# Kernel tuning notes

Hardware: AMD Instinct MI355X
Metric: run time of the kernel (lower is better)

## Reference

```python
import jax, jax.numpy as jnp
import numpy as np

DIM = 256
D_STATE = 16
D_CONV = 4
EXPAND = 2
D_INNER = DIM * EXPAND          # 512
DT_RANK = DIM // 16             # 16


def _dwconv(x_bcl, w, b, pad):
    # depthwise 1d conv; x_bcl: (B, C, L), w: (C, 1, K)
    out = jax.lax.conv_general_dilated(
        x_bcl, w, window_strides=(1,), padding=[pad],
        feature_group_count=x_bcl.shape[1],
        dimension_numbers=('NCH', 'OIH', 'NCH'))
    return out + b[None, :, None]


def _forward(x, ln_w, ln_b, W_in, conv_w, conv_b, W_xproj, W_dt, b_dt,
             A_log, D_ssm, W_outp, c1_w, c1_b, c2_w, c2_b, c3_w, c3_b,
             W_out, b_out, W_skip, b_skip):
    Bsz, C = x.shape[:2]
    img_dims = x.shape[2:]
    L = int(np.prod(img_dims))
    xf = x.reshape(Bsz, C, L).transpose(0, 2, 1)          # (B, L, C)
    # LayerNorm over channel dim
    mu = jnp.mean(xf, axis=-1, keepdims=True)
    var = jnp.var(xf, axis=-1, keepdims=True)
    xn = (xf - mu) / jnp.sqrt(var + 1e-5) * ln_w + ln_b   # (B, L, C)

    # ---------------- Mamba block ----------------
    xz = xn @ W_in.T                                      # (B, L, 2*Di)
    xi, z = jnp.split(xz, 2, axis=-1)
    k = conv_w.shape[-1]
    # causal depthwise conv (pad left d_conv-1, truncate to L), then silu
    xc = _dwconv(xi.transpose(0, 2, 1), conv_w, conv_b, (k - 1, 0))
    xc = jax.nn.silu(xc).transpose(0, 2, 1)               # (B, L, Di)
    x_dbl = xc @ W_xproj.T                                # (B, L, dt_rank + 2*N)
    dt = x_dbl[..., :DT_RANK]
    B_s = x_dbl[..., DT_RANK:DT_RANK + D_STATE]           # (B, L, N)
    C_s = x_dbl[..., DT_RANK + D_STATE:]                  # (B, L, N)
    delta = jax.nn.softplus(dt @ W_dt.T + b_dt)           # (B, L, Di)
    A = -jnp.exp(A_log)                                   # (Di, N)
    dA = jnp.exp(delta[..., None] * A)                    # (B, L, Di, N)
    dBu = (delta * xc)[..., None] * B_s[:, :, None, :]    # (B, L, Di, N)

    def step(h, inp):
        dA_t, dBu_t, c_t = inp
        h = dA_t * h + dBu_t                              # (B, Di, N)
        y = jnp.einsum('bdn,bn->bd', h, c_t)
        return h, y

    h0 = jnp.zeros((Bsz, D_INNER, D_STATE), dtype=x.dtype)
    _, ys = jax.lax.scan(
        step, h0,
        (dA.transpose(1, 0, 2, 3), dBu.transpose(1, 0, 2, 3), C_s.transpose(1, 0, 2)))
    y = ys.transpose(1, 0, 2) + D_ssm * xc                # (B, L, Di)
    y = y * jax.nn.silu(z)
    x_ssm = y @ W_outp.T                                  # (B, L, C)

    # ---------------- multi-scale depthwise convs ----------------
    xnT = xn.transpose(0, 2, 1)                           # (B, C, L)

    def msconv(w, b):
        kk = w.shape[-1]
        return jax.nn.silu(_dwconv(xnT, w, b, (kk // 2, kk // 2))).transpose(0, 2, 1)

    combined = x_ssm + msconv(c1_w, c1_b) + msconv(c2_w, c2_b) + msconv(c3_w, c3_b)
    out = combined @ W_out.T + b_out + xn @ W_skip.T + b_skip
    out = out.transpose(0, 2, 1).reshape(x.shape)
    return out + x


def setup_inputs() -> dict:
    key = jax.random.key(0)
    ks = jax.random.split(key, 12)

    def rn(k, shape, s=0.02):
        return jax.random.normal(k, shape, dtype=jnp.float32) * s

    return {
        'x': jax.random.normal(ks[0], (2, DIM, 64, 64), dtype=jnp.float32),
        'ln_w': jnp.ones((DIM,), jnp.float32),
        'ln_b': jnp.zeros((DIM,), jnp.float32),
        'W_in': rn(ks[1], (2 * D_INNER, DIM)),
        'conv_w': rn(ks[2], (D_INNER, 1, D_CONV), 0.1),
        'conv_b': jnp.zeros((D_INNER,), jnp.float32),
        'W_xproj': rn(ks[3], (DT_RANK + 2 * D_STATE, D_INNER)),
        'W_dt': rn(ks[4], (D_INNER, DT_RANK), 0.1),
        'b_dt': jnp.full((D_INNER,), -4.0, jnp.float32),  # softplus(-4) ~ 0.018, stable dt
        'A_log': jnp.log(jnp.broadcast_to(
            jnp.arange(1, D_STATE + 1, dtype=jnp.float32), (D_INNER, D_STATE))),
        'D_ssm': jnp.ones((D_INNER,), jnp.float32),
        'W_outp': rn(ks[5], (DIM, D_INNER)),
        'c1_w': rn(ks[6], (DIM, 1, 3), 0.1),
        'c1_b': jnp.zeros((DIM,), jnp.float32),
        'c2_w': rn(ks[7], (DIM, 1, 5), 0.1),
        'c2_b': jnp.zeros((DIM,), jnp.float32),
        'c3_w': rn(ks[8], (DIM, 1, 7), 0.1),
        'c3_b': jnp.zeros((DIM,), jnp.float32),
        'W_out': rn(ks[9], (DIM, DIM)),
        'b_out': jnp.zeros((DIM,), jnp.float32),
        'W_skip': rn(ks[10], (DIM, DIM)),
        'b_skip': jnp.zeros((DIM,), jnp.float32),
    }


def reference(x, ln_w, ln_b, W_in, conv_w, conv_b, W_xproj, W_dt, b_dt,
              A_log, D_ssm, W_outp, c1_w, c1_b, c2_w, c2_b, c3_w, c3_b,
              W_out, b_out, W_skip, b_skip):
    return _forward(x, ln_w, ln_b, W_in, conv_w, conv_b, W_xproj, W_dt, b_dt,
                    A_log, D_ssm, W_outp, c1_w, c1_b, c2_w, c2_b, c3_w, c3_b,
                    W_out, b_out, W_skip, b_skip)
```

## Files before the change

### kernel.cpp

```cpp
#include <hip/hip_runtime.h>
#include <hip/hip_bf16.h>
#include <math.h>
#include <cstddef>

#define BSZ 2
#define DM 256
#define LSEQ 4096
#define DIN 512
#define DXZ 1024
#define DS 16
#define RANK 16
#define GXP 48
#define LC 32
#define NC 128

typedef __attribute__((ext_vector_type(8))) short short8;
typedef __attribute__((ext_vector_type(4))) float f32x4;
struct bf4 { __hip_bfloat16 v[4]; };

__device__ __forceinline__ float silu_f(float x){ return x / (1.f + __expf(-x)); }
__device__ __forceinline__ float softplus_f(float x){ return fmaxf(x, 0.f) + log1pf(__expf(-fabsf(x))); }
__device__ __forceinline__ float b2f(__hip_bfloat16 v){ return __bfloat162float(v); }
__device__ __forceinline__ __hip_bfloat16 f2b(float v){ return __float2bfloat16(v); }

__device__ __forceinline__ void gl_lds16(const void* g, void* s){
    __builtin_amdgcn_global_load_lds((const __attribute__((address_space(1))) void*)g,
                                     (__attribute__((address_space(3))) void*)s, 16, 0, 0);
}

__global__ __launch_bounds__(256) void k_ln(const float* __restrict__ x,
                                            const float* __restrict__ lnw,
                                            const float* __restrict__ lnb,
                                            __hip_bfloat16* __restrict__ xnb){
    __shared__ float tile[DM * 33];
    __shared__ float rsum[8][32], rsq[8][32];
    __shared__ float mu_s[32], rs_s[32];
    int b  = blockIdx.x >> 7;
    int l0 = (blockIdx.x & 127) << 5;
    int tid = threadIdx.x;
    const float* xb = x + (size_t)b * DM * LSEQ;
    int lls = tid & 31, chi = tid >> 5;
    for (int cc = 0; cc < 32; ++cc){
        int c = cc * 8 + chi;
        tile[c * 33 + lls] = xb[(size_t)c * LSEQ + l0 + lls];
    }
    __syncthreads();
    int part = tid >> 5, l = tid & 31;
    float s = 0.f, sq = 0.f;
    for (int i = 0; i < 32; ++i){
        float v = tile[(part * 32 + i) * 33 + l];
        s += v; sq += v * v;
    }
    rsum[part][l] = s; rsq[part][l] = sq;
    __syncthreads();
    if (tid < 32){
        float ts = 0.f, tq = 0.f;
        for (int p = 0; p < 8; ++p){ ts += rsum[p][tid]; tq += rsq[p][tid]; }
        float mu  = ts * (1.f / DM);
        float var = tq * (1.f / DM) - mu * mu;
        mu_s[tid] = mu;
        rs_s[tid] = rsqrtf(var + 1e-5f);
    }
    __syncthreads();
    int c0 = tid & 63, lh = tid >> 6;
    for (int i = 0; i < 8; ++i){
        int ll = lh + 4 * i;
        float mu = mu_s[ll], rs = rs_s[ll];
        __hip_bfloat16* orow = xnb + (size_t)(b * LSEQ + l0 + ll) * 512;
        for (int j = 0; j < 4; ++j){
            int c = c0 + 64 * j;
            orow[c] = f2b((tile[c * 33 + ll] - mu) * rs * lnw[c] + lnb[c]);
        }
    }
}

__global__ __launch_bounds__(256) void k_cvtw(const float* __restrict__ W_in, const float* __restrict__ W_xproj,
                                              const float* __restrict__ W_outp, const float* __restrict__ W_out,
                                              const float* __restrict__ W_skip, const float* __restrict__ b_out,
                                              const float* __restrict__ b_skip,
                                              __hip_bfloat16* __restrict__ Winb, __hip_bfloat16* __restrict__ Wxpb,
                                              __hip_bfloat16* __restrict__ Wopb, __hip_bfloat16* __restrict__ Wcb,
                                              float* __restrict__ bc){
    int i0 = blockIdx.x * 256 + threadIdx.x;
    const int T = 256 * 256;
    for (int j = i0; j < 1024 * 256; j += T) Winb[j] = f2b(W_in[j]);
    for (int j = i0; j < 64 * 512; j += T){
        int r = j >> 9;
        Wxpb[j] = f2b(r < GXP ? W_xproj[r * 512 + (j & 511)] : 0.f);
    }
    for (int j = i0; j < 256 * 512; j += T) Wopb[j] = f2b(W_outp[j]);
    for (int j = i0; j < 256 * 512; j += T){
        int n = j >> 9, k = j & 511;
        Wcb[j] = f2b(k < 256 ? W_out[n * 256 + k] : W_skip[n * 256 + (k - 256)]);
    }
    if (i0 < 256) bc[i0] = b_out[i0] + b_skip[i0];
}

template<int EPI>
__global__ __launch_bounds__(256) void k_mgemm(const __hip_bfloat16* __restrict__ A, int lda,
                                               const __hip_bfloat16* __restrict__ W,
                                               const float* __restrict__ bias,
                                               void* __restrict__ Cv, int ldc,
                                               int N, int K){
    __shared__ __align__(16) __hip_bfloat16 As[128 * 64];
    __shared__ __align__(16) __hip_bfloat16 Ws[64 * 64];
    const int tid = threadIdx.x;
    const int wave = tid >> 6, lane = tid & 63;
    const int brow = blockIdx.x * 128, bcol = blockIdx.y * 64;
    const int wm = wave >> 1, wn = wave & 1;

    const int a_row = lane >> 3;
    const int a_chk = lane & 7;
    const int a_scol = ((a_chk ^ a_row) * 8);

    const int lrow = lane & 15;
    const int kc = lane >> 4;
    const int r7 = lrow & 7;

    f32x4 acc[4][2] = {};

    for (int k0 = 0; k0 < K; k0 += 64){
#pragma unroll
        for (int j = 0; j < 4; ++j){
            int seg = wave * 4 + j;
            const __hip_bfloat16* src = A + (size_t)(brow + seg * 8 + a_row) * lda + k0 + a_scol;
            gl_lds16(src, &As[seg * 512]);
        }
#pragma unroll
        for (int j = 0; j < 2; ++j){
            int seg = wave * 2 + j;
            const __hip_bfloat16* src = W + (size_t)(bcol + seg * 8 + a_row) * K + k0 + a_scol;
            gl_lds16(src, &Ws[seg * 512]);
        }
        __syncthreads();
#pragma unroll
        for (int kk = 0; kk < 2; ++kk){
            int kchunk = kk * 4 + kc;
            short8 af[4], bfr[2];
#pragma unroll
            for (int mi = 0; mi < 4; ++mi){
                int row = wm * 64 + mi * 16 + lrow;
                af[mi] = *(const short8*)&As[row * 64 + ((kchunk ^ r7) * 8)];
            }
#pragma unroll
            for (int ni = 0; ni < 2; ++ni){
                int row = wn * 32 + ni * 16 + lrow;
                bfr[ni] = *(const short8*)&Ws[row * 64 + ((kchunk ^ r7) * 8)];
            }
#pragma unroll
            for (int mi = 0; mi < 4; ++mi)
#pragma unroll
                for (int ni = 0; ni < 2; ++ni)
                    acc[mi][ni] = __builtin_amdgcn_mfma_f32_16x16x32_bf16(af[mi], bfr[ni], acc[mi][ni], 0, 0, 0);
        }
        __syncthreads();
    }

#pragma unroll
    for (int ni = 0; ni < 2; ++ni){
        int n = bcol + wn * 32 + ni * 16 + lrow;
        if (n >= N) continue;
        float bv = (EPI & 1) ? bias[n] : 0.f;
#pragma unroll
        for (int mi = 0; mi < 4; ++mi){
            int m0 = brow + wm * 64 + mi * 16 + kc * 4;
#pragma unroll
            for (int r = 0; r < 4; ++r){
                float v = acc[mi][ni][r] + bv;
                if (EPI & 8) ((__hip_bfloat16*)Cv)[(size_t)(m0 + r) * ldc + n] = f2b(v);
                else         ((float*)Cv)[(size_t)(m0 + r) * ldc + n] = v;
            }
        }
    }
}

__global__ __launch_bounds__(256) void k_dtgemm(const float* __restrict__ A, int lda,
                                                const float* __restrict__ Wt,
                                                const float* __restrict__ bias,
                                                __hip_bfloat16* __restrict__ C, int ldc){
    __shared__ float As[16][68];
    __shared__ float Ws[16][68];
    int bm = blockIdx.x * 64, bn = blockIdx.y * 64;
    int tid = threadIdx.x;
    int a_m = tid >> 2, a_k = (tid & 3) * 4;
    int tx = tid & 15, ty = tid >> 4;
    float acc[4][4] = {};
    {
        float4 av = *(const float4*)(A + (size_t)(bm + a_m) * lda + a_k);
        As[a_k + 0][a_m] = av.x; As[a_k + 1][a_m] = av.y;
        As[a_k + 2][a_m] = av.z; As[a_k + 3][a_m] = av.w;
        float4 wv = *(const float4*)(Wt + (size_t)(bn + a_m) * 16 + a_k);
        Ws[a_k + 0][a_m] = wv.x; Ws[a_k + 1][a_m] = wv.y;
        Ws[a_k + 2][a_m] = wv.z; Ws[a_k + 3][a_m] = wv.w;
        __syncthreads();
#pragma unroll
        for (int k = 0; k < 16; ++k){
            float4 a4 = *(const float4*)&As[k][ty * 4];
            float4 b4 = *(const float4*)&Ws[k][tx * 4];
            acc[0][0] += a4.x * b4.x; acc[0][1] += a4.x * b4.y; acc[0][2] += a4.x * b4.z; acc[0][3] += a4.x * b4.w;
            acc[1][0] += a4.y * b4.x; acc[1][1] += a4.y * b4.y; acc[1][2] += a4.y * b4.z; acc[1][3] += a4.y * b4.w;
            acc[2][0] += a4.z * b4.x; acc[2][1] += a4.z * b4.y; acc[2][2] += a4.z * b4.z; acc[2][3] += a4.z * b4.w;
            acc[3][0] += a4.w * b4.x; acc[3][1] += a4.w * b4.y; acc[3][2] += a4.w * b4.z; acc[3][3] += a4.w * b4.w;
        }
    }
    int n = bn + tx * 4;
    float4 bb = *(const float4*)(bias + n);
#pragma unroll
    for (int i = 0; i < 4; ++i){
        int m = bm + ty * 4 + i;
        __hip_bfloat16* cp = C + (size_t)m * ldc + n;
        cp[0] = f2b(softplus_f(acc[i][0] + bb.x));
        cp[1] = f2b(softplus_f(acc[i][1] + bb.y));
        cp[2] = f2b(softplus_f(acc[i][2] + bb.z));
        cp[3] = f2b(softplus_f(acc[i][3] + bb.w));
    }
}

__global__ __launch_bounds__(256) void k_conv(const __hip_bfloat16* __restrict__ xz,
                                              const float* __restrict__ cw,
                                              const float* __restrict__ cb,
                                              __hip_bfloat16* __restrict__ xc){
    int idx = blockIdx.x * 256 + threadIdx.x;
    int d4 = (idx & 127) * 4;
    int bl = idx >> 7;
    int l  = bl & (LSEQ - 1);
    const __hip_bfloat16* base = xz + (size_t)bl * DXZ + d4;
    float4 bias = *(const float4*)(cb + d4);
    float acc[4] = {bias.x, bias.y, bias.z, bias.w};
    float4 w0 = *(const float4*)(cw + (d4 + 0) * 4);
    float4 w1 = *(const float4*)(cw + (d4 + 1) * 4);
    float4 w2 = *(const float4*)(cw + (d4 + 2) * 4);
    float4 w3 = *(const float4*)(cw + (d4 + 3) * 4);
    const float* wj[4] = {(const float*)&w0, (const float*)&w1, (const float*)&w2, (const float*)&w3};
#pragma unroll
    for (int t = 0; t < 4; ++t){
        int ls = l - (3 - t);
        if (ls >= 0){
            bf4 v = *(const bf4*)(base - (size_t)(3 - t) * DXZ);
#pragma unroll
            for (int j = 0; j < 4; ++j) acc[j] += wj[j][t] * b2f(v.v[j]);
        }
    }
    bf4 o;
#pragma unroll
    for (int j = 0; j < 4; ++j) o.v[j] = f2b(silu_f(acc[j]));
    *(bf4*)(xc + (size_t)bl * DIN + d4) = o;
}

__global__ __launch_bounds__(512) void k_scan1(const __hip_bfloat16* __restrict__ delta,
                                               const __hip_bfloat16* __restrict__ xc,
                                               const float* __restrict__ xdbl,
                                               const float* __restrict__ A_log,
                                               float* __restrict__ Acar,
                                               float* __restrict__ Bcar){
    int bx = blockIdx.x;
    int dh = bx & 1;
    int c  = (bx >> 1) & (NC - 1);
    int b  = bx >> 8;
    int tid = threadIdx.x;
    int dloc = tid >> 1, nh = tid & 1;
    int d = dh * 256 + dloc;
    int n0 = nh * 8;
    __shared__ float Bs[LC][DS];
    {
        int t = tid >> 4, n = tid & 15;
        Bs[t][n] = xdbl[(size_t)(b * LSEQ + c * LC + t) * GXP + RANK + n];
    }
    __syncthreads();
    float Av[8];
    float a1 = -__expf(A_log[d * 16]);
    bool fast = true;
#pragma unroll
    for (int j = 0; j < 8; ++j){
        Av[j] = -__expf(A_log[d * 16 + n0 + j]);
        fast = fast && (fabsf(Av[j] - (float)(n0 + j + 1) * a1) <= 1e-4f * fabsf(Av[j]) + 1e-7f);
    }
    float ap[8], ac[8];
#pragma unroll
    for (int j = 0; j < 8; ++j){ ap[j] = 1.f; ac[j] = 0.f; }
    const __hip_bfloat16* dp = delta + (size_t)(b * LSEQ + c * LC) * DIN + d;
    const __hip_bfloat16* xp = xc    + (size_t)(b * LSEQ + c * LC) * DIN + d;
    if (fast){
        for (int t = 0; t < LC; ++t){
            float de = b2f(dp[(size_t)t * DIN]);
            float u  = de * b2f(xp[(size_t)t * DIN]);
            float p  = __expf(de * a1);
            float p2 = p * p, p4 = p2 * p2, p8 = p4 * p4;
            float da = nh ? p8 * p : p;
#pragma unroll
            for (int j = 0; j < 8; ++j){
                ap[j] *= da;
                ac[j] = da * ac[j] + u * Bs[t][n0 + j];
                da *= p;
            }
        }
    } else {
        for (int t = 0; t < LC; ++t){
            float de = b2f(dp[(size_t)t * DIN]);
            float u  = de * b2f(xp[(size_t)t * DIN]);
#pragma unroll
            for (int j = 0; j < 8; ++j){
                float da = __expf(de * Av[j]);
                ap[j] *= da;
                ac[j] = da * ac[j] + u * Bs[t][n0 + j];
            }
        }
    }
    size_t o = (size_t)c * (BSZ * DIN * 16) + (size_t)(b * DIN + d) * 16 + n0;
    *(float4*)(Acar + o)     = make_float4(ap[0], ap[1], ap[2], ap[3]);
    *(float4*)(Acar + o + 4) = make_float4(ap[4], ap[5], ap[6], ap[7]);
    *(float4*)(Bcar + o)     = make_float4(ac[0], ac[1], ac[2], ac[3]);
    *(float4*)(Bcar + o + 4) = make_float4(ac[4], ac[5], ac[6], ac[7]);
}

__global__ __launch_bounds__(128) void k_scan2(const float* __restrict__ Acar,
                                               const float* __restrict__ Bcar,
                                               float* __restrict__ hinit){
    int idx = blockIdx.x * 128 + threadIdx.x;
    const int STRIDE = BSZ * DIN * 16;
    float h = 0.f;
    for (int c = 0; c < NC; c += 4){
        size_t o0 = (size_t)c * STRIDE + idx;
        float a0 = Acar[o0], b0 = Bcar[o0];
        float a1 = Acar[o0 + STRIDE], b1 = Bcar[o0 + STRIDE];
        float a2 = Acar[o0 + 2 * STRIDE], b2 = Bcar[o0 + 2 * STRIDE];
        float a3 = Acar[o0 + 3 * STRIDE], b3 = Bcar[o0 + 3 * STRIDE];
        hinit[o0] = h;               h = a0 * h + b0;
        hinit[o0 + STRIDE] = h;      h = a1 * h + b1;
        hinit[o0 + 2 * STRIDE] = h;  h = a2 * h + b2;
        hinit[o0 + 3 * STRIDE] = h;  h = a3 * h + b3;
    }
}

__global__ __launch_bounds__(512) void k_scan3(const __hip_bfloat16* __restrict__ delta,
                                               const __hip_bfloat16* __restrict__ xc,
                                               const __hip_bfloat16* __restrict__ xz,
                                               const float* __restrict__ xdbl,
                                               const float* __restrict__ A_log,
                                               const float* __restrict__ D_ssm,
                                               const float* __restrict__ hinit,
                                               __hip_bfloat16* __restrict__ y){
    int bx = blockIdx.x;
    int dh = bx & 1;
    int c  = (bx >> 1) & (NC - 1);
    int b  = bx >> 8;
    int tid = threadIdx.x;
    int dloc = tid >> 1, nh = tid & 1;
    int d = dh * 256 + dloc;
    int n0 = nh * 8;
    __shared__ float Bs[LC][DS], Cs[LC][DS];
    {
        int t = tid >> 4, n = tid & 15;
        size_t r = (size_t)(b * LSEQ + c * LC + t) * GXP;
        Bs[t][n] = xdbl[r + RANK + n];
        Cs[t][n] = xdbl[r + RANK + DS + n];
    }
    __syncthreads();
    float Av[8];
    float a1 = -__expf(A_log[d * 16]);
    bool fast = true;
#pragma unroll
    for (int j = 0; j < 8; ++j){
        Av[j] = -__expf(A_log[d * 16 + n0 + j]);
        fast = fast && (fabsf(Av[j] - (float)(n0 + j + 1) * a1) <= 1e-4f * fabsf(Av[j]) + 1e-7f);
    }
    float h[8];
    size_t ho = (size_t)c * (BSZ * DIN * 16) + (size_t)(b * DIN + d) * 16 + n0;
    {
        float4 h0 = *(const float4*)(hinit + ho);
        float4 h1 = *(const float4*)(hinit + ho + 4);
        h[0] = h0.x; h[1] = h0.y; h[2] = h0.z; h[3] = h0.w;
        h[4] = h1.x; h[5] = h1.y; h[6] = h1.z; h[7] = h1.w;
    }
    float Dd = D_ssm[d];
    size_t rb = (size_t)(b * LSEQ + c * LC);
    if (fast){
        for (int t = 0; t < LC; ++t){
            size_t row = rb + t;
            float de  = b2f(delta[row * DIN + d]);
            float xcv = b2f(xc[row * DIN + d]);
            float u = de * xcv;
            float p  = __expf(de * a1);
            float p2 = p * p, p4 = p2 * p2, p8 = p4 * p4;
            float da = nh ? p8 * p : p;
            float yv = 0.f;
#pragma unroll
            for (int j = 0; j < 8; ++j){
                h[j] = da * h[j] + u * Bs[t][n0 + j];
                yv += h[j] * Cs[t][n0 + j];
                da *= p;
            }
            yv += __shfl_xor(yv, 1);
            if (nh == 0){
                float zv = b2f(xz[row * DXZ + DIN + d]);
                y[row * DIN + d] = f2b((yv + Dd * xcv) * silu_f(zv));
            }
        }
    } else {
        for (int t = 0; t < LC; ++t){
            size_t row = rb + t;
            float de  = b2f(delta[row * DIN + d]);
            float xcv = b2f(xc[row * DIN + d]);
            float u = de * xcv;
            float yv = 0.f;
#pragma unroll
            for (int j = 0; j < 8; ++j){
                float da = __expf(de * Av[j]);
                h[j] = da * h[j] + u * Bs[t][n0 + j];
                yv += h[j] * Cs[t][n0 + j];
            }
            yv += __shfl_xor(yv, 1);
            if (nh == 0){
                float zv = b2f(xz[row * DXZ + DIN + d]);
                y[row * DIN + d] = f2b((yv + Dd * xcv) * silu_f(zv));
            }
        }
    }
}

__global__ __launch_bounds__(256) void k_msconv(const __hip_bfloat16* __restrict__ xnb,
                                                const __hip_bfloat16* __restrict__ xssm,
                                                const float* __restrict__ c1w, const float* __restrict__ c1b,
                                                const float* __restrict__ c2w, const float* __restrict__ c2b,
                                                const float* __restrict__ c3w, const float* __restrict__ c3b,
                                                __hip_bfloat16* __restrict__ Acomb){
    int idx = blockIdx.x * 256 + threadIdx.x;
    int cch = idx & (DM - 1);
    int bl  = idx >> 8;
    int l   = bl & (LSEQ - 1);
    int bL  = bl - l;
    float a1 = c1b[cch], a2 = c2b[cch], a3 = c3b[cch];
#pragma unroll
    for (int j = -3; j <= 3; ++j){
        int ll = l + j;
        if ((unsigned)ll < LSEQ){
            float v = b2f(xnb[(size_t)(bL + ll) * 512 + cch]);
            if (j >= -1 && j <= 1) a1 += c1w[cch * 3 + (j + 1)] * v;
            if (j >= -2 && j <= 2) a2 += c2w[cch * 5 + (j + 2)] * v;
            a3 += c3w[cch * 7 + (j + 3)] * v;
        }
    }
    float res = b2f(xssm[(size_t)bl * 256 + cch]) + silu_f(a1) + silu_f(a2) + silu_f(a3);
    Acomb[(size_t)bl * 512 + cch] = f2b(res);
}

__global__ __launch_bounds__(256) void k_out(const float* __restrict__ outlc,
                                             const float* __restrict__ x,
                                             float* __restrict__ out){
    __shared__ float tile[32][33];
    int bid = blockIdx.x;
    int lt = bid & 127;
    int ct = (bid >> 7) & 7;
    int b  = bid >> 10;
    int l0 = lt * 32, c0 = ct * 32;
    int tx = threadIdx.x & 31, ty = threadIdx.x >> 5;
    for (int r = 0; r < 32; r += 8)
        tile[ty + r][tx] = outlc[(size_t)(b * LSEQ + l0 + ty + r) * DM + c0 + tx];
    __syncthreads();
    for (int r = 0; r < 32; r += 8){
        int cc = c0 + ty + r;
        size_t o = (size_t)(b * DM + cc) * LSEQ + l0 + tx;
        out[o] = tile[tx][ty + r] + x[o];
    }
}

extern "C" void kernel_launch(void* const* d_in, const int* in_sizes, int n_in,
                              void* d_out, int out_size, void* d_ws, size_t ws_size,
                              hipStream_t stream){
    const float* x      = (const float*)d_in[0];
    const float* ln_w   = (const float*)d_in[1];
    const float* ln_b   = (const float*)d_in[2];
    const float* W_in   = (const float*)d_in[3];
    const float* conv_w = (const float*)d_in[4];
    const float* conv_b = (const float*)d_in[5];
    const float* W_xproj= (const float*)d_in[6];
    const float* W_dt   = (const float*)d_in[7];
    const float* b_dt   = (const float*)d_in[8];
    const float* A_log  = (const float*)d_in[9];
    const float* D_ssm  = (const float*)d_in[10];
    const float* W_outp = (const float*)d_in[11];
    const float* c1_w   = (const float*)d_in[12];
    const float* c1_b   = (const float*)d_in[13];
    const float* c2_w   = (const float*)d_in[14];
    const float* c2_b   = (const float*)d_in[15];
    const float* c3_w   = (const float*)d_in[16];
    const float* c3_b   = (const float*)d_in[17];
    const float* W_out  = (const float*)d_in[18];
    const float* b_out  = (const float*)d_in[19];
    const float* W_skip = (const float*)d_in[20];
    const float* b_skip = (const float*)d_in[21];
    float* out = (float*)d_out;

    char* base = (char*)d_ws;
    const size_t MB = 1024 * 1024;
    __hip_bfloat16* Acomb = (__hip_bfloat16*)(base);
    __hip_bfloat16* xzb   = (__hip_bfloat16*)(base + 8*MB);
    __hip_bfloat16* xcb   = (__hip_bfloat16*)(base + 24*MB);
    float*          xdbl  = (float*)        (base + 32*MB);
    __hip_bfloat16* deltab= (__hip_bfloat16*)(base + 34*MB);
    float*          Acar  = (float*)        (base + 42*MB);
    float*          Bcar  = (float*)        (base + 50*MB);
    float*          hinit = (float*)        (base + 58*MB);
    __hip_bfloat16* xssmb = (__hip_bfloat16*)(base + 66*MB);
    __hip_bfloat16* Winb  = (__hip_bfloat16*)(base + 70*MB);
    __hip_bfloat16* Wxpb  = (__hip_bfloat16*)(base + 70*MB + 512*1024);
    __hip_bfloat16* Wopb  = (__hip_bfloat16*)(base + 71*MB);
    __hip_bfloat16* Wcb   = (__hip_bfloat16*)(base + 71*MB + 256*1024);
    float*          bc    = (float*)        (base + 71*MB + 512*1024);
    __hip_bfloat16* xnb   = Acomb + 256;
    __hip_bfloat16* ybf   = (__hip_bfloat16*)Bcar;
    float*          outlc = Acar;

    const int M = BSZ * LSEQ;

    k_cvtw<<<dim3(256), dim3(256), 0, stream>>>(W_in, W_xproj, W_outp, W_out, W_skip, b_out, b_skip,
                                                Winb, Wxpb, Wopb, Wcb, bc);
    k_ln<<<dim3(256), dim3(256), 0, stream>>>(x, ln_w, ln_b, xnb);
    k_mgemm<8><<<dim3(64, 16), dim3(256), 0, stream>>>(xnb, 512, Winb, nullptr, xzb, DXZ, 1024, 256);
    k_conv<<<dim3(M * DIN / 4 / 256), dim3(256), 0, stream>>>(xzb, conv_w, conv_b, xcb);
    k_mgemm<0><<<dim3(64, 1), dim3(256), 0, stream>>>(xcb, 512, Wxpb, nullptr, xdbl, GXP, GXP, 512);
    k_dtgemm<<<dim3(128, 8), dim3(256), 0, stream>>>(xdbl, GXP, W_dt, b_dt, deltab, DIN);
    k_scan1<<<dim3(BSZ * NC * 2), dim3(512), 0, stream>>>(deltab, xcb, xdbl, A_log, Acar, Bcar);
    k_scan2<<<dim3(128), dim3(128), 0, stream>>>(Acar, Bcar, hinit);
    k_scan3<<<dim3(BSZ * NC * 2), dim3(512), 0, stream>>>(deltab, xcb, xzb, xdbl, A_log, D_ssm, hinit, ybf);
    k_mgemm<8><<<dim3(64, 4), dim3(256), 0, stream>>>(ybf, 512, Wopb, nullptr, xssmb, 256, 256, 512);
    k_msconv<<<dim3(M * DM / 256), dim3(256), 0, stream>>>(xnb, xssmb, c1_w, c1_b, c2_w, c2_b, c3_w, c3_b, Acomb);
    k_mgemm<1><<<dim3(64, 4), dim3(256), 0, stream>>>(Acomb, 512, Wcb, bc, outlc, DM, 256, 512);
    k_out<<<dim3(2048), dim3(256), 0, stream>>>(outlc, x, out);
}
```

Baseline: 259.5 us.

## Parallelize chunk-carry scan with warp prefix scan and shrink x_proj GEMM tiles

The serial carry-propagation kernel, which used only 128 blocks of 128 threads each walking all 128 chunks in sequence, becomes a block-level parallel prefix scan. Each block stages a 128x32 slice of carries in LDS, pairs chunks, and runs a wavefront shuffle scan of the affine recurrence. The x_proj GEMM is also templated on block rows and launched with 32-row tiles, giving 256 blocks instead of 64 to fill more CUs. The parallel scan reorders the floating-point work, and the smaller GEMM tiles reuse less data per block.

```diff
diff --git a/kernel.cpp b/kernel.cpp
--- a/kernel.cpp
+++ b/kernel.cpp
@@ -13,6 +13,7 @@
 #define GXP 48
 #define LC 32
 #define NC 128
+#define CSTRIDE (BSZ * DIN * 16)
 
 typedef __attribute__((ext_vector_type(8))) short short8;
 typedef __attribute__((ext_vector_type(4))) float f32x4;
@@ -96,17 +97,21 @@
     if (i0 < 256) bc[i0] = b_out[i0] + b_skip[i0];
 }
 
-template<int EPI>
+template<int EPI, int BM = 128>
 __global__ __launch_bounds__(256) void k_mgemm(const __hip_bfloat16* __restrict__ A, int lda,
                                                const __hip_bfloat16* __restrict__ W,
                                                const float* __restrict__ bias,
                                                void* __restrict__ Cv, int ldc,
                                                int N, int K){
-    __shared__ __align__(16) __hip_bfloat16 As[128 * 64];
+    constexpr int SA = BM / 8;
+    constexpr int SAW = SA / 4;
+    constexpr int WROWS = BM / 2;
+    constexpr int MI = WROWS / 16;
+    __shared__ __align__(16) __hip_bfloat16 As[BM * 64];
     __shared__ __align__(16) __hip_bfloat16 Ws[64 * 64];
     const int tid = threadIdx.x;
     const int wave = tid >> 6, lane = tid & 63;
-    const int brow = blockIdx.x * 128, bcol = blockIdx.y * 64;
+    const int brow = blockIdx.x * BM, bcol = blockIdx.y * 64;
     const int wm = wave >> 1, wn = wave & 1;
 
     const int a_row = lane >> 3;
@@ -117,12 +122,12 @@
     const int kc = lane >> 4;
     const int r7 = lrow & 7;
 
-    f32x4 acc[4][2] = {};
+    f32x4 acc[MI][2] = {};
 
     for (int k0 = 0; k0 < K; k0 += 64){
 #pragma unroll
-        for (int j = 0; j < 4; ++j){
-            int seg = wave * 4 + j;
+        for (int j = 0; j < SAW; ++j){
+            int seg = wave * SAW + j;
             const __hip_bfloat16* src = A + (size_t)(brow + seg * 8 + a_row) * lda + k0 + a_scol;
             gl_lds16(src, &As[seg * 512]);
         }
@@ -136,10 +141,10 @@
 #pragma unroll
         for (int kk = 0; kk < 2; ++kk){
             int kchunk = kk * 4 + kc;
-            short8 af[4], bfr[2];
-#pragma unroll
-            for (int mi = 0; mi < 4; ++mi){
-                int row = wm * 64 + mi * 16 + lrow;
+            short8 af[MI], bfr[2];
+#pragma unroll
+            for (int mi = 0; mi < MI; ++mi){
+                int row = wm * WROWS + mi * 16 + lrow;
                 af[mi] = *(const short8*)&As[row * 64 + ((kchunk ^ r7) * 8)];
             }
 #pragma unroll
@@ -148,7 +153,7 @@
                 bfr[ni] = *(const short8*)&Ws[row * 64 + ((kchunk ^ r7) * 8)];
             }
 #pragma unroll
-            for (int mi = 0; mi < 4; ++mi)
+            for (int mi = 0; mi < MI; ++mi)
 #pragma unroll
                 for (int ni = 0; ni < 2; ++ni)
                     acc[mi][ni] = __builtin_amdgcn_mfma_f32_16x16x32_bf16(af[mi], bfr[ni], acc[mi][ni], 0, 0, 0);
@@ -162,8 +167,8 @@
         if (n >= N) continue;
         float bv = (EPI & 1) ? bias[n] : 0.f;
 #pragma unroll
-        for (int mi = 0; mi < 4; ++mi){
-            int m0 = brow + wm * 64 + mi * 16 + kc * 4;
+        for (int mi = 0; mi < MI; ++mi){
+            int m0 = brow + wm * WROWS + mi * 16 + kc * 4;
 #pragma unroll
             for (int r = 0; r < 4; ++r){
                 float v = acc[mi][ni][r] + bv;
@@ -306,29 +311,53 @@
             }
         }
     }
-    size_t o = (size_t)c * (BSZ * DIN * 16) + (size_t)(b * DIN + d) * 16 + n0;
+    size_t o = (size_t)c * CSTRIDE + (size_t)(b * DIN + d) * 16 + n0;
     *(float4*)(Acar + o)     = make_float4(ap[0], ap[1], ap[2], ap[3]);
     *(float4*)(Acar + o + 4) = make_float4(ap[4], ap[5], ap[6], ap[7]);
     *(float4*)(Bcar + o)     = make_float4(ac[0], ac[1], ac[2], ac[3]);
     *(float4*)(Bcar + o + 4) = make_float4(ac[4], ac[5], ac[6], ac[7]);
 }
 
-__global__ __launch_bounds__(128) void k_scan2(const float* __restrict__ Acar,
+__global__ __launch_bounds__(256) void k_scan2(const float* __restrict__ Acar,
                                                const float* __restrict__ Bcar,
                                                float* __restrict__ hinit){
-    int idx = blockIdx.x * 128 + threadIdx.x;
-    const int STRIDE = BSZ * DIN * 16;
-    float h = 0.f;
-    for (int c = 0; c < NC; c += 4){
-        size_t o0 = (size_t)c * STRIDE + idx;
-        float a0 = Acar[o0], b0 = Bcar[o0];
-        float a1 = Acar[o0 + STRIDE], b1 = Bcar[o0 + STRIDE];
-        float a2 = Acar[o0 + 2 * STRIDE], b2 = Bcar[o0 + 2 * STRIDE];
-        float a3 = Acar[o0 + 3 * STRIDE], b3 = Bcar[o0 + 3 * STRIDE];
-        hinit[o0] = h;               h = a0 * h + b0;
-        hinit[o0 + STRIDE] = h;      h = a1 * h + b1;
-        hinit[o0 + 2 * STRIDE] = h;  h = a2 * h + b2;
-        hinit[o0 + 3 * STRIDE] = h;  h = a3 * h + b3;
+    __shared__ float a_s[NC][33];
+    __shared__ float b_s[NC][33];
+    __shared__ float h_s[NC][33];
+    const int tid = threadIdx.x;
+    const int idx0 = blockIdx.x * 32;
+    const int s_ld = tid & 31, cr = tid >> 5;
+#pragma unroll
+    for (int r = 0; r < 16; ++r){
+        int c = r * 8 + cr;
+        size_t g = (size_t)c * CSTRIDE + idx0 + s_ld;
+        a_s[c][s_ld] = Acar[g];
+        b_s[c][s_ld] = Bcar[g];
+    }
+    __syncthreads();
+    const int lane = tid & 63, w = tid >> 6;
+#pragma unroll
+    for (int i = 0; i < 8; ++i){
+        int s = w * 8 + i;
+        float a0 = a_s[2 * lane][s],     b0 = b_s[2 * lane][s];
+        float a1 = a_s[2 * lane + 1][s], b1 = b_s[2 * lane + 1][s];
+        float av = a0 * a1, bv = a1 * b0 + b1;
+#pragma unroll
+        for (int d2 = 1; d2 < 64; d2 <<= 1){
+            float ao = __shfl_up(av, d2);
+            float bo = __shfl_up(bv, d2);
+            if (lane >= d2){ bv = av * bo + bv; av = ao * av; }
+        }
+        float ax = __shfl_up(av, 1), bx = __shfl_up(bv, 1);
+        if (lane == 0){ ax = 1.f; bx = 0.f; }
+        h_s[2 * lane][s]     = bx;
+        h_s[2 * lane + 1][s] = a0 * bx + b0;
+    }
+    __syncthreads();
+#pragma unroll
+    for (int r = 0; r < 16; ++r){
+        int c = r * 8 + cr;
+        hinit[(size_t)c * CSTRIDE + idx0 + s_ld] = h_s[c][s_ld];
     }
 }
 
@@ -365,7 +394,7 @@
         fast = fast && (fabsf(Av[j] - (float)(n0 + j + 1) * a1) <= 1e-4f * fabsf(Av[j]) + 1e-7f);
     }
     float h[8];
-    size_t ho = (size_t)c * (BSZ * DIN * 16) + (size_t)(b * DIN + d) * 16 + n0;
+    size_t ho = (size_t)c * CSTRIDE + (size_t)(b * DIN + d) * 16 + n0;
     {
         float4 h0 = *(const float4*)(hinit + ho);
         float4 h1 = *(const float4*)(hinit + ho + 4);
@@ -518,10 +547,10 @@
     k_ln<<<dim3(256), dim3(256), 0, stream>>>(x, ln_w, ln_b, xnb);
     k_mgemm<8><<<dim3(64, 16), dim3(256), 0, stream>>>(xnb, 512, Winb, nullptr, xzb, DXZ, 1024, 256);
     k_conv<<<dim3(M * DIN / 4 / 256), dim3(256), 0, stream>>>(xzb, conv_w, conv_b, xcb);
-    k_mgemm<0><<<dim3(64, 1), dim3(256), 0, stream>>>(xcb, 512, Wxpb, nullptr, xdbl, GXP, GXP, 512);
+    k_mgemm<0, 32><<<dim3(256, 1), dim3(256), 0, stream>>>(xcb, 512, Wxpb, nullptr, xdbl, GXP, GXP, 512);
     k_dtgemm<<<dim3(128, 8), dim3(256), 0, stream>>>(xdbl, GXP, W_dt, b_dt, deltab, DIN);
     k_scan1<<<dim3(BSZ * NC * 2), dim3(512), 0, stream>>>(deltab, xcb, xdbl, A_log, Acar, Bcar);
-    k_scan2<<<dim3(128), dim3(128), 0, stream>>>(Acar, Bcar, hinit);
+    k_scan2<<<dim3(512), dim3(256), 0, stream>>>(Acar, Bcar, hinit);
     k_scan3<<<dim3(BSZ * NC * 2), dim3(512), 0, stream>>>(deltab, xcb, xzb, xdbl, A_log, D_ssm, hinit, ybf);
     k_mgemm<8><<<dim3(64, 4), dim3(256), 0, stream>>>(ybf, 512, Wopb, nullptr, xssmb, 256, 256, 512);
     k_msconv<<<dim3(M * DM / 256), dim3(256), 0, stream>>>(xnb, xssmb, c1_w, c1_b, c2_w, c2_b, c3_w, c3_b, Acomb);
```

After: 250.2 us. 1.04x faster.
